# Performance work log

Measured on AMD Instinct MI355X. Metric: run time of the kernel, lower is better.

Reference implementation:

```python
import jax, jax.numpy as jnp
import numpy as np

N, IN, OUT, T = 65536, 256, 256, 8


def setup_inputs() -> dict:
    key = jax.random.key(0)
    k1, k2, k3, k4 = jax.random.split(key, 4)
    x = jax.random.normal(k1, (N, IN), dtype=jnp.float32)
    types = jax.random.randint(k2, (N,), 0, T, dtype=jnp.int32)
    # xavier_uniform for W: limit = sqrt(6 / (fan_in + fan_out)) with fan computed
    # on the last two dims (out_size, in_size)
    limit = float(np.sqrt(6.0 / (IN + OUT)))
    W = jax.random.uniform(k3, (T, OUT, IN), dtype=jnp.float32, minval=-limit, maxval=limit)
    # original inits b to zeros; use small random values so the bias path is exercised
    b = 0.01 * jax.random.normal(k4, (T, OUT), dtype=jnp.float32)
    return {"x": x, "types": types, "W": W, "b": b}


def reference(x, types, W, b):
    # out[i] = W[types[i]] @ x[i] + b[types[i]]
    # Grouped-GEMM expressed as a loop over the small fixed set of types,
    # avoiding the huge [N, OUT, IN] gather of W[types].
    num_types = W.shape[0]
    out = b[types]  # [N, OUT]
    for t in range(num_types):
        mask = (types == t)[:, None]  # [N, 1]
        out = out + jnp.where(mask, x @ W[t].T, jnp.float32(0.0))
    return out
```

## Files before the change

### kernel.cpp

```cpp
#include <hip/hip_runtime.h>
#include <stdint.h>


#define NROWS 65536
#define NTYPES 8
#define KDIM 256
#define ODIM 256
#define BM 32
#define MAX_TILES (NROWS / BM + NTYPES)

typedef __attribute__((ext_vector_type(8))) short short8;
typedef __attribute__((ext_vector_type(4))) float f32x4;

__device__ __forceinline__ unsigned short f2bf(float f) {
    unsigned int u = __float_as_uint(f);
    u += 0x7fffu + ((u >> 16) & 1u);
    return (unsigned short)(u >> 16);
}

__global__ void prep_bucket_kernel(const float* __restrict__ W,
                                   unsigned short* __restrict__ Wp,
                                   const int* __restrict__ types,
                                   int* __restrict__ cnt,
                                   int* __restrict__ idx) {
    const int b = blockIdx.x;
    if (b < 256) {
        const int gid = b * 256 + threadIdx.x;
        const int R   = gid >> 5;
        const int c32 = gid & 31;
        const int t  = R >> 8;
        const int r  = R & 255;
        const int f  = r >> 4;
        const int rr = r & 15;
        const int q  = c32 >> 2;
        const int l  = (c32 & 3) * 16 + rr;
        const float* src = W + (size_t)R * KDIM + c32 * 8;
        const float4 v0 = *(const float4*)src;
        const float4 v1 = *(const float4*)(src + 4);
        ushort4 p0, p1;
        p0.x = f2bf(v0.x); p0.y = f2bf(v0.y); p0.z = f2bf(v0.z); p0.w = f2bf(v0.w);
        p1.x = f2bf(v1.x); p1.y = f2bf(v1.y); p1.z = f2bf(v1.z); p1.w = f2bf(v1.w);
        ushort4* dst = (ushort4*)(Wp + (size_t)(((t * 16 + f) * 8 + q) * 512 + l * 8));
        dst[0] = p0; dst[1] = p1;
    } else {
        __shared__ int h[NTYPES];
        __shared__ int base[NTYPES];
        int i = (b - 256) * 256 + threadIdx.x;
        if (threadIdx.x < NTYPES) h[threadIdx.x] = 0;
        __syncthreads();
        int t = types[i];
        int r = atomicAdd(&h[t], 1);
        __syncthreads();
        if (threadIdx.x < NTYPES)
            base[threadIdx.x] = atomicAdd(&cnt[threadIdx.x], h[threadIdx.x]);
        __syncthreads();
        idx[t * NROWS + base[t] + r] = i;
    }
}

__global__ __launch_bounds__(256, 4)
void gemm_kernel(const float* __restrict__ x,
                 const float* __restrict__ bias,
                 const unsigned short* __restrict__ Wp,
                 const int* __restrict__ cnt,
                 const int* __restrict__ idx,
                 float* __restrict__ out) {
    const int bid = blockIdx.x;
    int t = -1, m0 = 0, count = 0, accum = 0;
    #pragma unroll
    for (int i = 0; i < NTYPES; ++i) {
        int c = cnt[i];
        int ntile = (c + BM - 1) / BM;
        if (t < 0 && bid < accum + ntile) { t = i; m0 = (bid - accum) * BM; count = c; }
        accum += ntile;
    }
    if (t < 0) return;

    __shared__ unsigned short As[BM * KDIM];
    __shared__ int idx_s[BM];
    char* AsB = (char*)As;

    const int tid = threadIdx.x;
    const int wave = tid >> 6;
    const int lane = tid & 63;
    const int lr = lane & 15;
    const int lq = lane >> 4;

    const unsigned short* wbase =
        Wp + (size_t)t * (16 * 8 * 512) + (size_t)(wave * 4) * 8 * 512 + lane * 8;
    short8 bf[3][4];
    #pragma unroll
    for (int j = 0; j < 4; ++j)
        bf[0][j] = *(const short8*)(wbase + j * 4096 + 0 * 512);
    #pragma unroll
    for (int j = 0; j < 4; ++j)
        bf[1][j] = *(const short8*)(wbase + j * 4096 + 1 * 512);

    float bv[4];
    #pragma unroll
    for (int j = 0; j < 4; ++j)
        bv[j] = bias[t * ODIM + wave * 64 + j * 16 + lr];

    {
        const int srow = tid >> 3;
        const int sc   = tid & 7;
        const int gr = m0 + srow;
        const int xr = idx[t * NROWS + (gr < count ? gr : count - 1)];
        if (sc == 0) idx_s[srow] = xr;
        const float* xs = x + (size_t)xr * KDIM;
        float4 av[8];
        #pragma unroll
        for (int s = 0; s < 8; ++s)
            av[s] = *(const float4*)(xs + (s * 8 + sc) * 4);
        #pragma unroll
        for (int s = 0; s < 8; ++s) {
            const int slot = s * 8 + sc;
            ushort4 pk;
            pk.x = f2bf(av[s].x); pk.y = f2bf(av[s].y);
            pk.z = f2bf(av[s].z); pk.w = f2bf(av[s].w);
            const int c = slot >> 1;
            *(ushort4*)(AsB + srow * 512 + ((c ^ (srow & 7)) * 16) + (slot & 1) * 8) = pk;
        }
    }
    __syncthreads();

    f32x4 acc[2][4] = {};

    #pragma unroll
    for (int q = 0; q < 8; ++q) {
        if (q < 6) {
            #pragma unroll
            for (int j = 0; j < 4; ++j)
                bf[(q + 2) % 3][j] =
                    *(const short8*)(wbase + j * 4096 + (q + 2) * 512);
        }
        short8 af[2];
        #pragma unroll
        for (int i = 0; i < 2; ++i) {
            const int row = i * 16 + lr;
            af[i] = *(const short8*)(AsB + row * 512
                                         + (((q << 2) + lq) ^ (row & 7)) * 16);
        }
        #pragma unroll
        for (int i = 0; i < 2; ++i)
            #pragma unroll
            for (int j = 0; j < 4; ++j)
                acc[i][j] = __builtin_amdgcn_mfma_f32_16x16x32_bf16(
                    af[i], bf[q % 3][j], acc[i][j], 0, 0, 0);
    }

    #pragma unroll
    for (int i = 0; i < 2; ++i) {
        #pragma unroll
        for (int r = 0; r < 4; ++r) {
            const int lm = i * 16 + lq * 4 + r;
            const int gr = m0 + lm;
            if (gr < count) {
                const size_t orow = (size_t)idx_s[lm] * ODIM;
                #pragma unroll
                for (int j = 0; j < 4; ++j)
                    out[orow + wave * 64 + j * 16 + lr] = acc[i][j][r] + bv[j];
            }
        }
    }
}

extern "C" void kernel_launch(void* const* d_in, const int* in_sizes, int n_in,
                              void* d_out, int out_size, void* d_ws, size_t ws_size,
                              hipStream_t stream) {
    const float* x     = (const float*)d_in[0];
    const int*   types = (const int*)d_in[1];
    const float* W     = (const float*)d_in[2];
    const float* b     = (const float*)d_in[3];
    float* out = (float*)d_out;

    char* ws = (char*)d_ws;
    int* cnt = (int*)ws;
    int* idx = (int*)(ws + 1024);
    unsigned short* Wp = (unsigned short*)(ws + 1024 + (size_t)NTYPES * NROWS * sizeof(int));

    hipMemsetAsync(cnt, 0, NTYPES * sizeof(int), stream);
    prep_bucket_kernel<<<512, 256, 0, stream>>>(W, Wp, types, cnt, idx);
    gemm_kernel<<<MAX_TILES, 256, 0, stream>>>(x, b, Wp, cnt, idx, out);
}
```

Before: 139.1 us.

## Precompute tile plan in separate kernel and preload all weight fragments upfront

After: 141.1 us. About the same (+1.4%).

```diff
diff --git a/kernel.cpp b/kernel.cpp
--- a/kernel.cpp
+++ b/kernel.cpp
@@ -58,23 +58,39 @@
     }
 }
 
-__global__ __launch_bounds__(256, 4)
+__global__ void plan_kernel(const int* __restrict__ cnt, int2* __restrict__ plan) {
+    __shared__ int start[NTYPES + 1];
+    if (threadIdx.x == 0) {
+        int acc = 0;
+        for (int t = 0; t < NTYPES; ++t) {
+            start[t] = acc;
+            acc += (cnt[t] + BM - 1) / BM;
+        }
+        start[NTYPES] = acc;
+    }
+    __syncthreads();
+    #pragma unroll
+    for (int t = 0; t < NTYPES; ++t) {
+        const int s = start[t], e = start[t + 1], c = cnt[t];
+        for (int i = s + (int)threadIdx.x; i < e; i += 256)
+            plan[i] = make_int2((((i - s) * BM) << 4) | t, c);
+    }
+    for (int i = start[NTYPES] + (int)threadIdx.x; i < MAX_TILES; i += 256)
+        plan[i] = make_int2(-1, 0);
+}
+
+__global__ __launch_bounds__(256, 2)
 void gemm_kernel(const float* __restrict__ x,
                  const float* __restrict__ bias,
                  const unsigned short* __restrict__ Wp,
-                 const int* __restrict__ cnt,
+                 const int2* __restrict__ plan,
                  const int* __restrict__ idx,
                  float* __restrict__ out) {
-    const int bid = blockIdx.x;
-    int t = -1, m0 = 0, count = 0, accum = 0;
-    #pragma unroll
-    for (int i = 0; i < NTYPES; ++i) {
-        int c = cnt[i];
-        int ntile = (c + BM - 1) / BM;
-        if (t < 0 && bid < accum + ntile) { t = i; m0 = (bid - accum) * BM; count = c; }
-        accum += ntile;
-    }
-    if (t < 0) return;
+    const int2 pe = plan[blockIdx.x];
+    if (pe.x < 0) return;
+    const int t = pe.x & 15;
+    const int m0 = pe.x >> 4;
+    const int count = pe.y;
 
     __shared__ unsigned short As[BM * KDIM];
     __shared__ int idx_s[BM];
@@ -88,13 +104,13 @@
 
     const unsigned short* wbase =
         Wp + (size_t)t * (16 * 8 * 512) + (size_t)(wave * 4) * 8 * 512 + lane * 8;
-    short8 bf[3][4];
+    short8 bf[8][4];
     #pragma unroll
-    for (int j = 0; j < 4; ++j)
-        bf[0][j] = *(const short8*)(wbase + j * 4096 + 0 * 512);
-    #pragma unroll
-    for (int j = 0; j < 4; ++j)
-        bf[1][j] = *(const short8*)(wbase + j * 4096 + 1 * 512);
+    for (int q = 0; q < 8; ++q)
+        #pragma unroll
+        for (int j = 0; j < 4; ++j)
+            bf[q][j] = *(const short8*)(wbase + j * 4096 + q * 512);
+    __builtin_amdgcn_sched_barrier(0);
 
     float bv[4];
     #pragma unroll
@@ -128,12 +144,6 @@
 
     #pragma unroll
     for (int q = 0; q < 8; ++q) {
-        if (q < 6) {
-            #pragma unroll
-            for (int j = 0; j < 4; ++j)
-                bf[(q + 2) % 3][j] =
-                    *(const short8*)(wbase + j * 4096 + (q + 2) * 512);
-        }
         short8 af[2];
         #pragma unroll
         for (int i = 0; i < 2; ++i) {
@@ -146,7 +156,7 @@
             #pragma unroll
             for (int j = 0; j < 4; ++j)
                 acc[i][j] = __builtin_amdgcn_mfma_f32_16x16x32_bf16(
-                    af[i], bf[q % 3][j], acc[i][j], 0, 0, 0);
+                    af[i], bf[q][j], acc[i][j], 0, 0, 0);
     }
 
     #pragma unroll
@@ -176,10 +186,12 @@
 
     char* ws = (char*)d_ws;
     int* cnt = (int*)ws;
-    int* idx = (int*)(ws + 1024);
-    unsigned short* Wp = (unsigned short*)(ws + 1024 + (size_t)NTYPES * NROWS * sizeof(int));
+    int2* plan = (int2*)(ws + 256);
+    int* idx = (int*)(ws + 32768);
+    unsigned short* Wp = (unsigned short*)(ws + 32768 + (size_t)NTYPES * NROWS * sizeof(int));
 
     hipMemsetAsync(cnt, 0, NTYPES * sizeof(int), stream);
     prep_bucket_kernel<<<512, 256, 0, stream>>>(W, Wp, types, cnt, idx);
-    gemm_kernel<<<MAX_TILES, 256, 0, stream>>>(x, b, Wp, cnt, idx, out);
+    plan_kernel<<<1, 256, 0, stream>>>(cnt, plan);
+    gemm_kernel<<<MAX_TILES, 256, 0, stream>>>(x, b, Wp, plan, idx, out);
 }
```
